# Performance work log

Measured on AMD Instinct MI355X. Metric: run time of the kernel, lower is better.

The kernel has to match this reference:

```python
import jax, jax.numpy as jnp
import numpy as np
import math

HEADS, LANDMARKS, PINV_ITERS, RES_K = 8, 256, 6, 33
DIM = 512


def layer_norm(x, g, b, eps=1e-5):
    mu = x.mean(-1, keepdims=True)
    var = ((x - mu) ** 2).mean(-1, keepdims=True)
    return (x - mu) * jax.lax.rsqrt(var + eps) * g + b


def iter_pinv(x, iters=PINV_ITERS):
    # Moore-Penrose pseudo-inverse via Newton-Schulz-like iteration (lucidrains nystrom-attention)
    ax = jnp.abs(x)
    z = jnp.swapaxes(x, -1, -2) / (jnp.max(ax.sum(-1)) * jnp.max(ax.sum(-2)))
    I = jnp.eye(x.shape[-1], dtype=x.dtype)
    for _ in range(iters):
        xz = x @ z
        z = 0.25 * z @ (13.0 * I - xz @ (15.0 * I - xz @ (7.0 * I - xz)))
    return z


def nystrom_attention(x, qkv_w, out_w, out_b, res_w):
    b, n, dim = x.shape
    h, m = HEADS, LANDMARKS
    d = dim // h
    pad = (m - n % m) % m
    xp = jnp.pad(x, ((0, 0), (pad, 0), (0, 0)))  # pad at sequence start (as in original)
    npad = n + pad
    qkv = xp @ qkv_w  # [b, npad, 3*dim]
    q, k, v = jnp.split(qkv, 3, axis=-1)
    q, k, v = (t.reshape(b, npad, h, d).transpose(0, 2, 1, 3) for t in (q, k, v))
    q = q * (d ** -0.5)
    l = npad // m
    q_l = q.reshape(b, h, m, l, d).mean(3)  # [b,h,m,d] landmarks
    k_l = k.reshape(b, h, m, l, d).mean(3)
    attn1 = jax.nn.softmax(jnp.einsum('bhid,bhjd->bhij', q, k_l), axis=-1)    # [b,h,npad,m]
    attn2 = jax.nn.softmax(jnp.einsum('bhid,bhjd->bhij', q_l, k_l), axis=-1)  # [b,h,m,m]
    attn3 = jax.nn.softmax(jnp.einsum('bhid,bhjd->bhij', q_l, k), axis=-1)    # [b,h,m,npad]
    out = (attn1 @ iter_pinv(attn2)) @ (attn3 @ v)  # [b,h,npad,d]
    # depthwise residual conv over sequence dim: v as NCHW = [b, heads, npad, d], kernel (33,1)
    res = jax.lax.conv_general_dilated(
        v, res_w, window_strides=(1, 1), padding=((RES_K // 2, RES_K // 2), (0, 0)),
        dimension_numbers=('NCHW', 'OIHW', 'NCHW'), feature_group_count=h)
    out = out + res
    out = out.transpose(0, 2, 1, 3).reshape(b, npad, dim)
    out = out @ out_w + out_b  # dropout is identity at eval
    return out[:, -n:]


def dwconv(x, w, b, k):
    y = jax.lax.conv_general_dilated(
        x, w, (1, 1), ((k // 2, k // 2), (k // 2, k // 2)),
        dimension_numbers=('NCHW', 'OIHW', 'NCHW'), feature_group_count=x.shape[1])
    return y + b[None, :, None, None]


def ppeg(x, H, W, w7, b7, w5, b5, w3, b3):
    B, _, C = x.shape
    cls_tok, feat = x[:, :1], x[:, 1:]
    cnn = feat.transpose(0, 2, 1).reshape(B, C, H, W)
    y = cnn + dwconv(cnn, w7, b7, 7) + dwconv(cnn, w5, b5, 5) + dwconv(cnn, w3, b3, 3)
    y = y.reshape(B, C, H * W).transpose(0, 2, 1)
    return jnp.concatenate([cls_tok, y], axis=1)


def _forward(features, fc1_w, fc1_b, cls_token,
             l1_norm_g, l1_norm_b, l1_qkv_w, l1_out_w, l1_out_b, l1_res_w,
             ppeg_w7, ppeg_b7, ppeg_w5, ppeg_b5, ppeg_w3, ppeg_b3,
             l2_norm_g, l2_norm_b, l2_qkv_w, l2_out_w, l2_out_b, l2_res_w,
             norm_g, norm_b, fc2_w, fc2_b):
    h = jax.nn.relu(features @ fc1_w + fc1_b)  # [B, N, 512]
    B, N, D = h.shape
    _H = _W = int(math.ceil(math.sqrt(N)))
    add_length = _H * _W - N
    h = jnp.concatenate([h, h[:, :add_length, :]], axis=1)  # square pad by wraparound
    h = jnp.concatenate([jnp.broadcast_to(cls_token, (B, 1, D)), h], axis=1)
    h = h + nystrom_attention(layer_norm(h, l1_norm_g, l1_norm_b), l1_qkv_w, l1_out_w, l1_out_b, l1_res_w)
    h = ppeg(h, _H, _W, ppeg_w7, ppeg_b7, ppeg_w5, ppeg_b5, ppeg_w3, ppeg_b3)
    h = h + nystrom_attention(layer_norm(h, l2_norm_g, l2_norm_b), l2_qkv_w, l2_out_w, l2_out_b, l2_res_w)
    h = layer_norm(h, norm_g, norm_b)[:, 0]
    return h @ fc2_w + fc2_b  # [B, num_classes]


def setup_inputs() -> dict:
    key = jax.random.key(0)
    ks = jax.random.split(key, 32)
    B, N, F, D = 2, 16000, 1024, DIM
    s = 0.02
    def rn(k, shape, scale=s):
        return jax.random.normal(k, shape, dtype=jnp.float32) * scale
    inp = {
        'features': jax.random.normal(ks[0], (B, N, F), dtype=jnp.float32),
        'fc1_w': rn(ks[1], (F, D)), 'fc1_b': jnp.zeros((D,), jnp.float32),
        'cls_token': rn(ks[2], (1, 1, D), 1.0),
        'l1_norm_g': jnp.ones((D,), jnp.float32), 'l1_norm_b': jnp.zeros((D,), jnp.float32),
        'l1_qkv_w': rn(ks[3], (D, 3 * D)),
        'l1_out_w': rn(ks[4], (D, D)), 'l1_out_b': jnp.zeros((D,), jnp.float32),
        'l1_res_w': rn(ks[5], (HEADS, 1, RES_K, 1)),
        'ppeg_w7': rn(ks[6], (D, 1, 7, 7)), 'ppeg_b7': jnp.zeros((D,), jnp.float32),
        'ppeg_w5': rn(ks[7], (D, 1, 5, 5)), 'ppeg_b5': jnp.zeros((D,), jnp.float32),
        'ppeg_w3': rn(ks[8], (D, 1, 3, 3)), 'ppeg_b3': jnp.zeros((D,), jnp.float32),
        'l2_norm_g': jnp.ones((D,), jnp.float32), 'l2_norm_b': jnp.zeros((D,), jnp.float32),
        'l2_qkv_w': rn(ks[9], (D, 3 * D)),
        'l2_out_w': rn(ks[10], (D, D)), 'l2_out_b': jnp.zeros((D,), jnp.float32),
        'l2_res_w': rn(ks[11], (HEADS, 1, RES_K, 1)),
        'norm_g': jnp.ones((D,), jnp.float32), 'norm_b': jnp.zeros((D,), jnp.float32),
        'fc2_w': rn(ks[12], (D, 1)), 'fc2_b': jnp.zeros((1,), jnp.float32),
    }
    return inp


def reference(features, fc1_w, fc1_b, cls_token,
              l1_norm_g, l1_norm_b, l1_qkv_w, l1_out_w, l1_out_b, l1_res_w,
              ppeg_w7, ppeg_b7, ppeg_w5, ppeg_b5, ppeg_w3, ppeg_b3,
              l2_norm_g, l2_norm_b, l2_qkv_w, l2_out_w, l2_out_b, l2_res_w,
              norm_g, norm_b, fc2_w, fc2_b):
    return _forward(features, fc1_w, fc1_b, cls_token,
                    l1_norm_g, l1_norm_b, l1_qkv_w, l1_out_w, l1_out_b, l1_res_w,
                    ppeg_w7, ppeg_b7, ppeg_w5, ppeg_b5, ppeg_w3, ppeg_b3,
                    l2_norm_g, l2_norm_b, l2_qkv_w, l2_out_w, l2_out_b, l2_res_w,
                    norm_g, norm_b, fc2_w, fc2_b)
```

## Files before the change

### kernel.cpp

```cpp
#include <hip/hip_runtime.h>
#include <math.h>

#define NTOK 16130
#define NPAD 16384
#define PADF 254
#define NB   2
#define DM   512
#define NH   8
#define HD   64
#define LM   256
#define SEG  64

typedef __attribute__((ext_vector_type(8))) short short8v;
typedef __attribute__((ext_vector_type(4))) float f32x4;
typedef __attribute__((ext_vector_type(2))) float f32x2;
typedef unsigned int u32;

__device__ __forceinline__ float wred_max(float v){
  #pragma unroll
  for(int o=32;o;o>>=1) v=fmaxf(v,__shfl_xor(v,o));
  return v;
}
__device__ __forceinline__ float wred_sum(float v){
  #pragma unroll
  for(int o=32;o;o>>=1) v+=__shfl_xor(v,o);
  return v;
}
__device__ __forceinline__ float block_max256(float v, float* s4){
  v=wred_max(v);
  if((threadIdx.x&63)==0) s4[threadIdx.x>>6]=v;
  __syncthreads();
  v=fmaxf(fmaxf(s4[0],s4[1]),fmaxf(s4[2],s4[3]));
  __syncthreads();
  return v;
}
__device__ __forceinline__ float block_sum256(float v, float* s4){
  v=wred_sum(v);
  if((threadIdx.x&63)==0) s4[threadIdx.x>>6]=v;
  __syncthreads();
  v=s4[0]+s4[1]+s4[2]+s4[3];
  __syncthreads();
  return v;
}
__device__ __forceinline__ unsigned short f2bf(float f){
  unsigned u=__float_as_uint(f);
  u = u + 0x7FFFu + ((u>>16)&1u);
  return (unsigned short)(u>>16);
}
__device__ __forceinline__ float bf2f(unsigned short u){
  return __uint_as_float(((unsigned)u)<<16);
}
__device__ __forceinline__ unsigned cvtpk(float a, float b){
  unsigned r;
  asm("v_cvt_pk_bf16_f32 %0, %1, %2" : "=v"(r) : "v"(a), "v"(b));
  return r;
}
__device__ __forceinline__ void gl16(const unsigned short* g, unsigned short* l){
  __builtin_amdgcn_global_load_lds(
      (const __attribute__((address_space(1))) u32*)(g),
      (__attribute__((address_space(3))) u32*)(l), 16, 0, 0);
}

__global__ void k_f2bf4(const float* __restrict__ x, unsigned short* __restrict__ y, int n4){
  int i=blockIdx.x*256+threadIdx.x; if(i>=n4) return;
  float4 v=((const float4*)x)[i];
  ushort4 r; r.x=f2bf(v.x); r.y=f2bf(v.y); r.z=f2bf(v.z); r.w=f2bf(v.w);
  ((ushort4*)y)[i]=r;
}
__global__ __launch_bounds__(256) void k_wconv_t(
    const float* __restrict__ W, unsigned short* __restrict__ Wt, int K, int N){
  __shared__ float T[32][33];
  int k0=blockIdx.x*32, n0=blockIdx.y*32;
  int t=threadIdx.x, r=t>>3, c4=(t&7)*4;
  float4 a=*(const float4*)(W+(size_t)(k0+r)*N + n0+c4);
  T[r][c4]=a.x; T[r][c4+1]=a.y; T[r][c4+2]=a.z; T[r][c4+3]=a.w;
  __syncthreads();
  ushort4 w;
  w.x=f2bf(T[c4+0][r]); w.y=f2bf(T[c4+1][r]);
  w.z=f2bf(T[c4+2][r]); w.w=f2bf(T[c4+3][r]);
  *(ushort4*)(Wt+(size_t)(n0+r)*K + k0+c4)=w;
}

template<int MODE, int ASRC>
__global__ __launch_bounds__(256) void k_mfma_gemm(
    const void* __restrict__ Ap, const unsigned short* __restrict__ Bt,
    int M, int N, int K,
    const float* __restrict__ bias,
    void* __restrict__ o0, void* __restrict__ o1, void* __restrict__ o2)
{
  __shared__ __align__(16) unsigned short Sh[128*64];
  int t=threadIdx.x;
  int bx=blockIdx.x, by=blockIdx.y;
  {
    int gx=gridDim.x; int wg=by*gx+bx; int nwg=gx*gridDim.y;
    int cpx=nwg>>3; int x2=(wg&7)*cpx+(wg>>3);
    by=x2/gx; bx=x2-by*gx;
  }
  int row0=by*128, col0=bx*128;
  int lane=t&63, w=t>>6, wr=w>>1, wc=w&1, lr=lane&15, kg=lane>>4;
  f32x4 acc[4][4];
  #pragma unroll
  for(int m=0;m<4;m++)
    #pragma unroll
    for(int n=0;n<4;n++) acc[m][n]=(f32x4){0.f,0.f,0.f,0.f};

  for(int k0=0;k0<K;k0+=32){
    __syncthreads();
    #pragma unroll
    for(int i=0;i<2;i++){
      int flat=i*256+t, r=flat>>2, k8=flat&3;
      int kofs=k0+k8*8;
      const unsigned short* asrc;
      if constexpr(ASRC==0){
        asrc=(const unsigned short*)Ap+(size_t)(row0+r)*K+kofs;
      } else {
        int rr2=row0+r; int bb=rr2>>14, ri=rr2&16383;
        int head=kofs>>6, dd=kofs&63;
        asrc=(const unsigned short*)Ap + (((size_t)bb*NH+head)*NPAD+ri)*HD + dd;
      }
      gl16(asrc, Sh+(size_t)flat*8);
      gl16(Bt+(size_t)(col0+r)*K+kofs, Sh+4096+(size_t)flat*8);
    }
    __syncthreads();
    short8v af[4], bf[4];
    #pragma unroll
    for(int m=0;m<4;m++) af[m]=*(const short8v*)(Sh+(wr*64+m*16+lr)*32 + kg*8);
    #pragma unroll
    for(int n=0;n<4;n++) bf[n]=*(const short8v*)(Sh+4096+(wc*64+n*16+lr)*32 + kg*8);
    #pragma unroll
    for(int m=0;m<4;m++)
      #pragma unroll
      for(int n=0;n<4;n++)
        acc[m][n]=__builtin_amdgcn_mfma_f32_16x16x32_bf16(af[m],bf[n],acc[m][n],0,0,0);
  }
  if constexpr(MODE==1){
    #pragma unroll
    for(int p=0;p<2;p++){
      __syncthreads();
      #pragma unroll
      for(int mm=0;mm<2;mm++){
        int m=2*p+mm;
        #pragma unroll
        for(int n=0;n<4;n++){
          int cc=wc*64+n*16+lr;
          int c=col0+cc;
          float sc=((c>>9)==0)?0.125f:1.f;
          #pragma unroll
          for(int j=0;j<4;j++){
            int lrow=wr*32+mm*16+kg*4+j;
            Sh[lrow*128+cc]=f2bf(acc[m][n][j]*sc);
          }
        }
      }
      __syncthreads();
      #pragma unroll
      for(int i=0;i<4;i++){
        int p2=i*256+t;
        int r2=p2>>4, ck=p2&15;
        int grow=row0+(r2>>5)*64+(2*p+((r2>>4)&1))*16+(r2&15);
        int bb=grow>>14, rr=grow&16383;
        int c=col0+ck*8;
        int which=c>>9, hcol=c&511, head=hcol>>6, dd=hcol&63;
        unsigned short* dst=(which==0)?(unsigned short*)o0:
                            (which==1)?(unsigned short*)o1:(unsigned short*)o2;
        *(short8v*)(dst + (((size_t)bb*NH+head)*NPAD+rr)*HD+dd) =
            *(const short8v*)(Sh + r2*128 + ck*8);
      }
    }
  } else {
    #pragma unroll
    for(int m=0;m<4;m++){
      int rbase=row0 + wr*64 + m*16 + kg*4;
      #pragma unroll
      for(int j=0;j<4;j++){
        int r=rbase+j;
        #pragma unroll
        for(int n=0;n<4;n++){
          int c=col0 + wc*64 + n*16 + lr;
          float val=acc[m][n][j];
          if(MODE==0){
            float* h=(float*)o0;
            int bb=(r>=16000)?1:0, ii=r-bb*16000;
            float vv=fmaxf(val+bias[c],0.f);
            h[((size_t)bb*NTOK + 1 + ii)*DM + c]=vv;
            if(ii<129) h[((size_t)bb*NTOK + 16001 + ii)*DM + c]=vv;
          } else {
            float* h=(float*)o0;
            int bb=r>>14, rr=r&16383;
            if(rr>=PADF)
              h[((size_t)bb*NTOK + (rr-PADF))*DM + c]+=val+bias[c];
          }
        }
      }
    }
  }
}

__global__ void k_cls(const float* __restrict__ cls, float* __restrict__ h){
  int t=blockIdx.x*256+threadIdx.x;
  if(t<2*DM) h[(size_t)(t>>9)*NTOK*DM + (t&511)]=cls[t&511];
}

__global__ __launch_bounds__(256) void k_lnpad(
    const float* __restrict__ h, const float* __restrict__ g,
    const float* __restrict__ bta, unsigned short* __restrict__ xln)
{
  int wid=blockIdx.x*4+(threadIdx.x>>6);
  int lane=threadIdx.x&63;
  int bb=wid>>14, i=wid&16383;
  unsigned short* dst=xln+(size_t)wid*DM+lane*8;
  if(i<PADF){
    ushort4 z=(ushort4){0,0,0,0};
    *(ushort4*)dst=z; *(ushort4*)(dst+4)=z;
    return;
  }
  const float* src=h+((size_t)bb*NTOK + (i-PADF))*DM + lane*8;
  float4 v0=*(const float4*)src;
  float4 v1=*(const float4*)(src+4);
  float x[8]={v0.x,v0.y,v0.z,v0.w,v1.x,v1.y,v1.z,v1.w};
  float s=0.f;
  #pragma unroll
  for(int k=0;k<8;k++) s+=x[k];
  float mu=wred_sum(s)*(1.f/512.f);
  float d[8]; float vs=0.f;
  #pragma unroll
  for(int k=0;k<8;k++){ d[k]=x[k]-mu; vs+=d[k]*d[k]; }
  float rst=rsqrtf(wred_sum(vs)*(1.f/512.f)+1e-5f);
  float4 g0=*(const float4*)(g+lane*8),   g1=*(const float4*)(g+lane*8+4);
  float4 b0=*(const float4*)(bta+lane*8), b1=*(const float4*)(bta+lane*8+4);
  float gg[8]={g0.x,g0.y,g0.z,g0.w,g1.x,g1.y,g1.z,g1.w};
  float bb8[8]={b0.x,b0.y,b0.z,b0.w,b1.x,b1.y,b1.z,b1.w};
  ushort4 w0,w1;
  w0.x=f2bf(d[0]*rst*gg[0]+bb8[0]); w0.y=f2bf(d[1]*rst*gg[1]+bb8[1]);
  w0.z=f2bf(d[2]*rst*gg[2]+bb8[2]); w0.w=f2bf(d[3]*rst*gg[3]+bb8[3]);
  w1.x=f2bf(d[4]*rst*gg[4]+bb8[4]); w1.y=f2bf(d[5]*rst*gg[5]+bb8[5]);
  w1.z=f2bf(d[6]*rst*gg[6]+bb8[6]); w1.w=f2bf(d[7]*rst*gg[7]+bb8[7]);
  *(ushort4*)dst=w0; *(ushort4*)(dst+4)=w1;
}

__global__ void k_lmean2(const unsigned short* __restrict__ qsrc,
                         const unsigned short* __restrict__ ksrc,
                         float* __restrict__ qlf, unsigned short* __restrict__ qlb_,
                         float* __restrict__ klf, unsigned short* __restrict__ klb_){
  int gid=blockIdx.x;
  const unsigned short* src; float* dstf; unsigned short* dstb;
  if(gid<4096){ src=qsrc; dstf=qlf; dstb=qlb_; }
  else        { src=ksrc; dstf=klf; dstb=klb_; gid-=4096; }
  int bh=gid>>8, s=gid&255, d=threadIdx.x;
  const unsigned short* p=src + (((size_t)bh*NPAD)+s*SEG)*HD + d;
  float acc=0.f;
  #pragma unroll
  for(int l=0;l<SEG;l++) acc+=bf2f(p[(size_t)l*HD]);
  float m=acc*(1.f/64.f);
  dstf[((size_t)bh*LM+s)*HD+d]=m;
  dstb[((size_t)bh*LM+s)*HD+d]=f2bf(m);
}

__global__ __launch_bounds__(256) void k_vtrans(
    const unsigned short* __restrict__ v, unsigned short* __restrict__ vt)
{
  __shared__ unsigned short tile[64][72];
  int kt=blockIdx.x, bh=blockIdx.y;
  int t=threadIdx.x;
  int r=t>>2, sgq=t&3;
  const short8v* src=(const short8v*)(v + ((size_t)bh*NPAD + kt*64 + r)*HD + sgq*16);
  *(short8v*)(&tile[r][sgq*16])  =src[0];
  *(short8v*)(&tile[r][sgq*16+8])=src[1];
  __syncthreads();
  int d=t>>2;
  union{unsigned short u[16]; short8v v8[2];} pk;
  #pragma unroll
  for(int i=0;i<16;i++) pk.u[i]=tile[sgq*16+i][d];
  short8v* dst=(short8v*)(vt + ((size_t)bh*HD + d)*NPAD + kt*64 + sgq*16);
  dst[0]=pk.v8[0]; dst[1]=pk.v8[1];
}

__global__ __launch_bounds__(256) void k_attn2(
    const float* __restrict__ ql, const float* __restrict__ kl,
    float* __restrict__ attn2,
    unsigned short* __restrict__ a2h, unsigned short* __restrict__ a2l)
{
  __shared__ float qrow[64]; __shared__ float s4[4];
  int bh=blockIdx.x>>8, i=blockIdx.x&255, j=threadIdx.x;
  if(j<64) qrow[j]=ql[((size_t)bh*LM+i)*HD+j];
  __syncthreads();
  const float* kp=kl+((size_t)bh*LM+j)*HD;
  float l=0.f;
  #pragma unroll
  for(int d=0;d<64;d++) l+=qrow[d]*kp[d];
  float m=block_max256(l,s4);
  float e=__expf(l-m);
  float s=block_sum256(e,s4);
  float pv=e/s;
  size_t o=((size_t)bh*LM+i)*LM+j;
  attn2[o]=pv;
  unsigned short hh=f2bf(pv);
  a2h[o]=hh; a2l[o]=f2bf(pv-bf2f(hh));
}

__global__ void k_colsumA(const float* __restrict__ x, float* __restrict__ partial){
  int bh=blockIdx.y, ic=blockIdx.x, j=threadIdx.x;
  const float* p=x+(size_t)bh*65536+(size_t)ic*16*256;
  float s=0.f;
  #pragma unroll
  for(int i=0;i<16;i++) s+=p[(size_t)i*256+j];
  partial[((size_t)bh*16+ic)*256+j]=s;
}
__global__ void k_colsumB(const float* __restrict__ partial, float* __restrict__ cs){
  int bh=blockIdx.x, j=threadIdx.x;
  float s=0.f;
  #pragma unroll
  for(int ic=0;ic<16;ic++) s+=partial[((size_t)bh*16+ic)*256+j];
  cs[bh*256+j]=s;
}
__global__ void k_pinvscale(const float* __restrict__ cs, float* __restrict__ scale){
  __shared__ float s4[4];
  float mc=-1e30f;
  for(int i=threadIdx.x;i<4096;i+=256) mc=fmaxf(mc,cs[i]);
  mc=block_max256(mc,s4);
  if(threadIdx.x==0) scale[0]=1.f/mc;
}
__global__ __launch_bounds__(256) void k_zinit_hl(
    const float* __restrict__ x, const float* __restrict__ scale,
    unsigned short* __restrict__ zh, unsigned short* __restrict__ zl,
    unsigned short* __restrict__ zth, unsigned short* __restrict__ ztl){
  __shared__ float T1[32][33], T2[32][33];
  int bh=blockIdx.x>>6, tile=blockIdx.x&63;
  int i0=(tile>>3)*32, j0=(tile&7)*32;
  int t=threadIdx.x, r=t>>3, c4=(t&7)*4;
  size_t base=(size_t)bh*65536;
  float4 a=*(const float4*)(x+base+(size_t)(i0+r)*256+j0+c4);
  float4 b=*(const float4*)(x+base+(size_t)(j0+r)*256+i0+c4);
  T1[r][c4]=a.x; T1[r][c4+1]=a.y; T1[r][c4+2]=a.z; T1[r][c4+3]=a.w;
  T2[r][c4]=b.x; T2[r][c4+1]=b.y; T2[r][c4+2]=b.z; T2[r][c4+3]=b.w;
  __syncthreads();
  float s=scale[0];
  size_t o=base+(size_t)(i0+r)*256+j0+c4;
  ushort4 nh,nl,th,tl;
  {
    float vn, vt; unsigned short hh;
    vn=T2[c4+0][r]*s; hh=f2bf(vn); nh.x=hh; nl.x=f2bf(vn-bf2f(hh));
    vn=T2[c4+1][r]*s; hh=f2bf(vn); nh.y=hh; nl.y=f2bf(vn-bf2f(hh));
    vn=T2[c4+2][r]*s; hh=f2bf(vn); nh.z=hh; nl.z=f2bf(vn-bf2f(hh));
    vn=T2[c4+3][r]*s; hh=f2bf(vn); nh.w=hh; nl.w=f2bf(vn-bf2f(hh));
    vt=T1[r][c4+0]*s; hh=f2bf(vt); th.x=hh; tl.x=f2bf(vt-bf2f(hh));
    vt=T1[r][c4+1]*s; hh=f2bf(vt); th.y=hh; tl.y=f2bf(vt-bf2f(hh));
    vt=T1[r][c4+2]*s; hh=f2bf(vt); th.z=hh; tl.z=f2bf(vt-bf2f(hh));
    vt=T1[r][c4+3]*s; hh=f2bf(vt); th.w=hh; tl.w=f2bf(vt-bf2f(hh));
  }
  *(ushort4*)(zh+o)=nh; *(ushort4*)(zl+o)=nl;
  *(ushort4*)(zth+o)=th; *(ushort4*)(ztl+o)=tl;
}

template<int MODE, int PREC>
__global__ __launch_bounds__(256) void k_bmm3(
    const unsigned short* __restrict__ Ah, const unsigned short* __restrict__ Al,
    const unsigned short* __restrict__ Bth, const unsigned short* __restrict__ Btl,
    const unsigned short* __restrict__ Xh, const unsigned short* __restrict__ Xl,
    unsigned short* __restrict__ Cnh, unsigned short* __restrict__ Cnl,
    unsigned short* __restrict__ Cth, unsigned short* __restrict__ Ctl,
    int Ndim)
{
  __shared__ unsigned short AsH[32*136], BsH[64*136];
  __shared__ unsigned short AsL[PREC?32*136:8], BsL[PREC?64*136:8];
  int bh=blockIdx.z;
  int n0=blockIdx.x*64, m0=blockIdx.y*32;
  int t=threadIdx.x, lane=t&63, w=t>>6;
  int c=lane&15, g=lane>>4;
  int wr=(w>>1)*16, wc=(w&1)*32;
  f32x4 acc[2];
  acc[0]=(f32x4){0.f,0.f,0.f,0.f};
  acc[1]=(f32x4){0.f,0.f,0.f,0.f};
  size_t Abase=(size_t)bh*65536;
  size_t Bbase=(size_t)bh*(size_t)Ndim*256;
  int r=t>>3, k16=(t&7)*16;
  const unsigned short* ApH =Ah +Abase+(size_t)(m0+r)*256+k16;
  const unsigned short* BpH0=Bth+Bbase+(size_t)(n0+r)*256+k16;
  const unsigned short* BpH1=Bth+Bbase+(size_t)(n0+32+r)*256+k16;
  const unsigned short* ApL =Al +Abase+(size_t)(m0+r)*256+k16;
  const unsigned short* BpL0=Btl+Bbase+(size_t)(n0+r)*256+k16;
  const unsigned short* BpL1=Btl+Bbase+(size_t)(n0+32+r)*256+k16;
  short8v rah[2],rbh0[2],rbh1[2], ral[2],rbl0[2],rbl1[2];
  #pragma unroll
  for(int i=0;i<2;i++){
    rah[i] =*(const short8v*)(ApH +i*8);
    rbh0[i]=*(const short8v*)(BpH0+i*8);
    rbh1[i]=*(const short8v*)(BpH1+i*8);
    if constexpr(PREC==1){
      ral[i] =*(const short8v*)(ApL +i*8);
      rbl0[i]=*(const short8v*)(BpL0+i*8);
      rbl1[i]=*(const short8v*)(BpL1+i*8);
    }
  }
  int k0=0;
  for(;;){
    __syncthreads();
    #pragma unroll
    for(int i=0;i<2;i++){
      *(short8v*)(AsH + r*136 + k16 + i*8)=rah[i];
      *(short8v*)(BsH + r*136 + k16 + i*8)=rbh0[i];
      *(short8v*)(BsH + (r+32)*136 + k16 + i*8)=rbh1[i];
      if constexpr(PREC==1){
        *(short8v*)(AsL + r*136 + k16 + i*8)=ral[i];
        *(short8v*)(BsL + r*136 + k16 + i*8)=rbl0[i];
        *(short8v*)(BsL + (r+32)*136 + k16 + i*8)=rbl1[i];
      }
    }
    __syncthreads();
    int kn=k0+128;
    if(kn<256){
      #pragma unroll
      for(int i=0;i<2;i++){
        rah[i] =*(const short8v*)(ApH +kn+i*8);
        rbh0[i]=*(const short8v*)(BpH0+kn+i*8);
        rbh1[i]=*(const short8v*)(BpH1+kn+i*8);
        if constexpr(PREC==1){
          ral[i] =*(const short8v*)(ApL +kn+i*8);
          rbl0[i]=*(const short8v*)(BpL0+kn+i*8);
          rbl1[i]=*(const short8v*)(BpL1+kn+i*8);
        }
      }
    }
    #pragma unroll
    for(int ks=0;ks<4;ks++){
      short8v af=*(const short8v*)(AsH+(wr+c)*136 + ks*32 + g*8);
      short8v alf;
      if constexpr(PREC==1) alf=*(const short8v*)(AsL+(wr+c)*136 + ks*32 + g*8);
      #pragma unroll
      for(int nt=0;nt<2;nt++){
        short8v bf=*(const short8v*)(BsH+(wc+nt*16+c)*136 + ks*32 + g*8);
        acc[nt]=__builtin_amdgcn_mfma_f32_16x16x32_bf16(af,bf,acc[nt],0,0,0);
        if constexpr(PREC==1){
          short8v blf=*(const short8v*)(BsL+(wc+nt*16+c)*136 + ks*32 + g*8);
          acc[nt]=__builtin_amdgcn_mfma_f32_16x16x32_bf16(af,blf,acc[nt],0,0,0);
          acc[nt]=__builtin_amdgcn_mfma_f32_16x16x32_bf16(alf,bf,acc[nt],0,0,0);
        }
      }
    }
    if(kn>=256) break;
    k0=kn;
  }
  int rb=m0+wr+g*4;
  #pragma unroll
  for(int nt=0;nt<2;nt++){
    int cc=n0+wc+nt*16+c;
    float vv[4];
    #pragma unroll
    for(int j=0;j<4;j++){
      float a=acc[nt][j];
      int rr=rb+j;
      if(MODE==1){
        float xv=bf2f(Xh[Abase+(size_t)rr*256+cc])+bf2f(Xl[Abase+(size_t)rr*256+cc]);
        a=(rr==cc?15.f:0.f)-7.f*xv+a;
      } else if(MODE==2){
        a=(rr==cc?13.f:0.f)-a;
      } else if(MODE==3){
        a*=0.25f;
      }
      vv[j]=a;
    }
    if(MODE==0||MODE==3){
      #pragma unroll
      for(int j=0;j<4;j++){
        unsigned short hh=f2bf(vv[j]);
        Cnh[Abase+(size_t)(rb+j)*256+cc]=hh;
        Cnl[Abase+(size_t)(rb+j)*256+cc]=f2bf(vv[j]-bf2f(hh));
      }
    }
    {
      ushort4 hv, lv;
      hv.x=f2bf(vv[0]); hv.y=f2bf(vv[1]); hv.z=f2bf(vv[2]); hv.w=f2bf(vv[3]);
      lv.x=f2bf(vv[0]-bf2f(hv.x)); lv.y=f2bf(vv[1]-bf2f(hv.y));
      lv.z=f2bf(vv[2]-bf2f(hv.z)); lv.w=f2bf(vv[3]-bf2f(hv.w));
      size_t co=((size_t)bh*Ndim+cc)*256+rb;
      *(ushort4*)(Cth+co)=hv;
      if(MODE!=4) *(ushort4*)(Ctl+co)=lv;
    }
  }
}

__global__ __launch_bounds__(512) void k_attn3m(
    const unsigned short* __restrict__ qlb,
    const unsigned short* __restrict__ kb,
    const unsigned short* __restrict__ vtb,
    float* __restrict__ pacc, float* __restrict__ pms)
{
  __shared__ unsigned short Ks[64*72];
  __shared__ unsigned short Vs[64*72];
  int ck=blockIdx.x, rh=blockIdx.y, bh=blockIdx.z;
  int t=threadIdx.x, lane=t&63, w=t>>6;
  int c=lane&15, g=lane>>4;
  int qrow0=rh*128 + w*16;
  short8v Qf[2];
  #pragma unroll
  for(int kw=0;kw<2;kw++)
    Qf[kw]=*(const short8v*)(qlb + ((size_t)bh*LM + qrow0 + c)*HD + kw*32 + g*8);
  f32x4 accO[4];
  float mrun=-3e38f, srun=0.f;
  #pragma unroll
  for(int d=0;d<4;d++) accO[d]=(f32x4){0.f,0.f,0.f,0.f};
  int sr=t>>3, sgk=t&7;
  for(int sc=0;sc<16;++sc){
    int key0=ck*1024 + sc*64;
    __syncthreads();
    *(short8v*)(Ks + sr*72 + sgk*8) =
      *(const short8v*)(kb + ((size_t)bh*NPAD + key0 + sr)*HD + sgk*8);
    *(short8v*)(Vs + sr*72 + sgk*8) =
      *(const short8v*)(vtb + ((size_t)bh*HD + sr)*NPAD + key0 + sgk*8);
    __syncthreads();
    f32x4 s[4];
    #pragma unroll
    for(int mt=0;mt<4;mt++){
      short8v a0=*(const short8v*)(Ks + (mt*16+c)*72 + g*8);
      short8v a1=*(const short8v*)(Ks + (mt*16+c)*72 + 32 + g*8);
      f32x4 z=(f32x4){0.f,0.f,0.f,0.f};
      z=__builtin_amdgcn_mfma_f32_16x16x32_bf16(a0,Qf[0],z,0,0,0);
      z=__builtin_amdgcn_mfma_f32_16x16x32_bf16(a1,Qf[1],z,0,0,0);
      s[mt]=z;
    }
    unsigned U[4][2];
    {
      float cm=-3e38f;
      #pragma unroll
      for(int mt=0;mt<4;mt++)
        #pragma unroll
        for(int j=0;j<4;j++) cm=fmaxf(cm,s[mt][j]);
      cm=fmaxf(cm,__shfl_xor(cm,16));
      cm=fmaxf(cm,__shfl_xor(cm,32));
      float mnew=fmaxf(mrun,cm);
      float f=__expf(mrun-mnew);
      mrun=mnew;
      float ps=0.f;
      #pragma unroll
      for(int mt=0;mt<4;mt++){
        float p0=__expf(s[mt][0]-mnew);
        float p1=__expf(s[mt][1]-mnew);
        float p2=__expf(s[mt][2]-mnew);
        float p3=__expf(s[mt][3]-mnew);
        ps+=p0+p1+p2+p3;
        U[mt][0]=cvtpk(p0,p1);
        U[mt][1]=cvtpk(p2,p3);
      }
      ps+=__shfl_xor(ps,16); ps+=__shfl_xor(ps,32);
      srun=srun*f+ps;
      #pragma unroll
      for(int d=0;d<4;d++){
        accO[d][0]*=f; accO[d][1]*=f; accO[d][2]*=f; accO[d][3]*=f;
      }
    }
    #pragma unroll
    for(int kw=0;kw<2;kw++){
      union{unsigned u[4]; short8v v;} pk;
      #pragma unroll
      for(int wd=0;wd<4;wd++){
        int sl=c+16*(((g&1)<<1)+(wd>>1));
        unsigned va=(unsigned)__shfl((int)U[kw*2  ][wd&1],sl);
        unsigned vb=(unsigned)__shfl((int)U[kw*2+1][wd&1],sl);
        pk.u[wd]=(lane>=32)?vb:va;
      }
      #pragma unroll
      for(int d=0;d<4;d++){
        short8v vf=*(const short8v*)(Vs + (d*16+c)*72 + kw*32 + g*8);
        accO[d]=__builtin_amdgcn_mfma_f32_16x16x32_bf16(vf,pk.v,accO[d],0,0,0);
      }
    }
  }
  size_t pb=((size_t)bh*16+ck)*LM;
  int q=qrow0+c;
  #pragma unroll
  for(int d=0;d<4;d++)
    *(f32x4*)(pacc + (pb+q)*HD + d*16 + g*4)=accO[d];
  if(g==0){ pms[(pb+q)*2]=mrun; pms[(pb+q)*2+1]=srun; }
}
__global__ __launch_bounds__(256) void k_attn3vc(
    const float* __restrict__ pacc, const float* __restrict__ pms,
    unsigned short* __restrict__ a3vth, unsigned short* __restrict__ a3vtl)
{
  int gid=blockIdx.x*4+(threadIdx.x>>6);
  int bh=gid>>8, row=gid&255, lane=threadIdx.x&63;
  float M=-3e38f;
  float ms[16], ss[16];
  #pragma unroll
  for(int c=0;c<16;c++){
    size_t pb=((size_t)bh*16+c)*LM+row;
    ms[c]=pms[pb*2]; ss[c]=pms[pb*2+1];
    M=fmaxf(M,ms[c]);
  }
  float S=0.f,a=0.f;
  #pragma unroll
  for(int c=0;c<16;c++){
    float f=__expf(ms[c]-M);
    S+=ss[c]*f;
    a+=pacc[(((size_t)bh*16+c)*LM+row)*HD+lane]*f;
  }
  float v=a/S;
  unsigned short hi=f2bf(v);
  a3vth[((size_t)bh*HD+lane)*LM+row]=hi;
  a3vtl[((size_t)bh*HD+lane)*LM+row]=f2bf(v-bf2f(hi));
}

__global__ __launch_bounds__(512) void k_attn1m(
    const unsigned short* __restrict__ qb,
    const unsigned short* __restrict__ klb,
    const unsigned short* __restrict__ w2t,
    unsigned short* __restrict__ aohb)
{
  __shared__ unsigned short klS[256*72];
  __shared__ unsigned short w2S[64*264];
  int qt=blockIdx.x, bh=blockIdx.y;
  int t=threadIdx.x, lane=t&63, w=t>>6;
  int c=lane&15, g=lane>>4;
  {
    int r=t>>1, hf=t&1;
    const short8v* s=(const short8v*)(klb + ((size_t)bh*LM+r)*HD + hf*32);
    short8v* d=(short8v*)(klS + r*72 + hf*32);
    d[0]=s[0]; d[1]=s[1]; d[2]=s[2]; d[3]=s[3];
    int r2=t>>3, sg2=t&7;
    const short8v* s2=(const short8v*)(w2t + ((size_t)bh*HD+r2)*LM + sg2*32);
    short8v* d2=(short8v*)(w2S + r2*264 + sg2*32);
    d2[0]=s2[0]; d2[1]=s2[1]; d2[2]=s2[2]; d2[3]=s2[3];
  }
  __syncthreads();
  int q0=qt*256 + w*32;
  #pragma unroll
  for(int n=0;n<2;n++){
    const unsigned short* qrow=qb + ((size_t)bh*NPAD + q0 + n*16 + c)*HD;
    short8v qf0=*(const short8v*)(qrow + g*8);
    short8v qf1=*(const short8v*)(qrow + 32 + g*8);
    f32x4 s[16];
    #pragma unroll
    for(int mt=0;mt<16;mt++){
      short8v a0=*(const short8v*)(klS + (mt*16+c)*72 + g*8);
      short8v a1=*(const short8v*)(klS + (mt*16+c)*72 + 32 + g*8);
      f32x4 z=(f32x4){0.f,0.f,0.f,0.f};
      z=__builtin_amdgcn_mfma_f32_16x16x32_bf16(a0,qf0,z,0,0,0);
      z=__builtin_amdgcn_mfma_f32_16x16x32_bf16(a1,qf1,z,0,0,0);
      s[mt]=z;
    }
    float M=-3e38f;
    #pragma unroll
    for(int mt=0;mt<16;mt++)
      #pragma unroll
      for(int j=0;j<4;j++) M=fmaxf(M,s[mt][j]);
    M=fmaxf(M,__shfl_xor(M,16));
    M=fmaxf(M,__shfl_xor(M,32));
    float sum=0.f;
    unsigned U[16][2];
    #pragma unroll
    for(int mt=0;mt<16;mt++){
      float p0=__expf(s[mt][0]-M);
      float p1=__expf(s[mt][1]-M);
      float p2=__expf(s[mt][2]-M);
      float p3=__expf(s[mt][3]-M);
      sum+=p0+p1+p2+p3;
      U[mt][0]=cvtpk(p0,p1);
      U[mt][1]=cvtpk(p2,p3);
    }
    sum+=__shfl_xor(sum,16); sum+=__shfl_xor(sum,32);
    float inv=1.f/sum;
    f32x4 accO[4];
    #pragma unroll
    for(int d=0;d<4;d++) accO[d]=(f32x4){0.f,0.f,0.f,0.f};
    #pragma unroll
    for(int kw=0;kw<8;kw++){
      union{unsigned u[4]; short8v v;} pk;
      #pragma unroll
      for(int wd=0;wd<4;wd++){
        int sl=c+16*(((g&1)<<1)+(wd>>1));
        unsigned va=(unsigned)__shfl((int)U[kw*2  ][wd&1],sl);
        unsigned vb=(unsigned)__shfl((int)U[kw*2+1][wd&1],sl);
        pk.u[wd]=(lane>=32)?vb:va;
      }
      #pragma unroll
      for(int d=0;d<4;d++){
        short8v vf=*(const short8v*)(w2S + (d*16+c)*264 + kw*32 + g*8);
        accO[d]=__builtin_amdgcn_mfma_f32_16x16x32_bf16(vf,pk.v,accO[d],0,0,0);
      }
    }
    int q=q0+n*16+c;
    #pragma unroll
    for(int d=0;d<4;d++){
      f32x4 o=accO[d];
      uint2 pk2;
      pk2.x=cvtpk(o[0]*inv, o[1]*inv);
      pk2.y=cvtpk(o[2]*inv, o[3]*inv);
      *(uint2*)(aohb + ((size_t)bh*NPAD+q)*HD + d*16 + g*4)=pk2;
    }
  }
}

__global__ __launch_bounds__(256) void k_resconv2(
    const unsigned short* __restrict__ vt, const float* __restrict__ rw,
    unsigned short* __restrict__ aohb){
  int bx=blockIdx.x, bh=blockIdx.y;
  int t=threadIdx.x, d=t&63, g=t>>6;
  int i0=bx*32+g*8;
  int hh=bh&7;
  const unsigned short* vr=vt + ((size_t)bh*HD + d)*NPAD;
  float wv[40];
  int start=i0-16;
  if(start>=0 && start+40<=NPAD){
    #pragma unroll
    for(int b=0;b<5;b++){
      short8v v8=*(const short8v*)(vr+start+b*8);
      #pragma unroll
      for(int j=0;j<8;j++) wv[b*8+j]=bf2f((unsigned short)v8[j]);
    }
  } else {
    #pragma unroll
    for(int t2=0;t2<40;t2++){
      int src=start+t2;
      wv[t2]=(src>=0&&src<NPAD)?bf2f(vr[src]):0.f;
    }
  }
  const float* wt=rw+hh*33;
  #pragma unroll
  for(int p=0;p<8;p++){
    float a=0.f;
    #pragma unroll
    for(int tk=0;tk<33;tk++) a+=wv[p+tk]*wt[tk];
    size_t o=((size_t)bh*NPAD+i0+p)*HD+d;
    aohb[o]=f2bf(bf2f(aohb[o])+a);
  }
}

__global__ void k_wprep(const float* __restrict__ w7, const float* __restrict__ b7,
                        const float* __restrict__ w5, const float* __restrict__ b5,
                        const float* __restrict__ w3, const float* __restrict__ b3,
                        unsigned short* __restrict__ wcat){
  int t=blockIdx.x*256+threadIdx.x;
  if(t>=50*512) return;
  int r=t>>9, c=t&511;
  float v;
  if(r<49){
    int ky=r/7, kx=r%7;
    v=w7[(size_t)c*49+r];
    if(ky>=1&&ky<=5&&kx>=1&&kx<=5) v+=w5[(size_t)c*25+(ky-1)*5+(kx-1)];
    if(ky>=2&&ky<=4&&kx>=2&&kx<=4) v+=w3[(size_t)c*9+(ky-2)*3+(kx-2)];
  } else {
    v=b7[c]+b5[c]+b3[c];
  }
  wcat[t]=f2bf(v);
}

__global__ __launch_bounds__(256,4) void k_ppeg4(
    const float* __restrict__ src, const unsigned short* __restrict__ wcat,
    float* __restrict__ dst)
{
  __shared__ float patch[32][198];
  __shared__ float wsf[50][32];
  int bx=blockIdx.x;
  int cz=blockIdx.y, bb=blockIdx.z;
  int t=threadIdx.x, c=t&31, g=t>>5;
  int ty0=(bx>>4)*8, tx0=(bx&15)*8;
  const float* base=src+((size_t)bb*NTOK+1)*DM + cz*32 + c;
  #pragma unroll
  for(int i=0;i<25;i++){
    int p=g+8*i;
    if(p<196){
      int py=p/14, px=p%14;
      int yy=ty0-3+py, xx=tx0-3+px;
      float v=0.f;
      if(yy>=0&&yy<127&&xx>=0&&xx<127) v=base[(size_t)(yy*127+xx)*DM];
      patch[c][p]=v;
    }
  }
  #pragma unroll
  for(int i=0;i<7;i++){
    int r=g+8*i; if(r<50) wsf[r][c]=bf2f(wcat[(size_t)r*DM + cz*32 + c]);
  }
  __syncthreads();
  float bias=wsf[49][c];
  f32x2 acc2[4];
  #pragma unroll
  for(int j=0;j<4;j++){
    acc2[j][0]=patch[c][(g+3)*14+(j+3)]+bias;
    acc2[j][1]=patch[c][(g+3)*14+(j+7)]+bias;
  }
  #pragma unroll
  for(int ky=0;ky<7;ky++){
    float win[14];
    #pragma unroll
    for(int x2=0;x2<7;x2++){
      f32x2 wp=*(const f32x2*)(&patch[c][(g+ky)*14+2*x2]);
      win[2*x2]=wp[0]; win[2*x2+1]=wp[1];
    }
    #pragma unroll
    for(int kx=0;kx<7;kx++){
      float wv=wsf[ky*7+kx][c];
      f32x2 w2={wv,wv};
      #pragma unroll
      for(int j=0;j<4;j++){
        f32x2 v2={win[j+kx],win[j+4+kx]};
        acc2[j]=__builtin_elementwise_fma(v2,w2,acc2[j]);
      }
    }
  }
  int y=ty0+g;
  if(y<127){
    #pragma unroll
    for(int j=0;j<4;j++){
      int x=tx0+j;
      if(x<127)
        dst[((size_t)bb*NTOK+1+(size_t)(y*127+x))*DM + cz*32 + c]=acc2[j][0];
      int x4=tx0+j+4;
      if(x4<127)
        dst[((size_t)bb*NTOK+1+(size_t)(y*127+x4))*DM + cz*32 + c]=acc2[j][1];
    }
  }
}

__global__ void k_cpcls(const float* __restrict__ h, float* __restrict__ dst){
  int t=blockIdx.x*256+threadIdx.x;
  if(t<2*DM) dst[(size_t)(t>>9)*NTOK*DM + (t&511)]=h[(size_t)(t>>9)*NTOK*DM + (t&511)];
}

__global__ __launch_bounds__(256) void k_final(
    const float* __restrict__ h, const float* __restrict__ g, const float* __restrict__ bta,
    const float* __restrict__ w, const float* __restrict__ fb, float* __restrict__ out)
{
  int bb=blockIdx.x, t=threadIdx.x;
  const float* src=h+(size_t)bb*NTOK*DM;
  float x0=src[t], x1=src[t+256];
  __shared__ float s4[4];
  float mu=block_sum256(x0+x1,s4)*(1.f/512.f);
  float d0=x0-mu, d1=x1-mu;
  float var=block_sum256(d0*d0+d1*d1,s4)*(1.f/512.f);
  float rst=rsqrtf(var+1e-5f);
  float y0=d0*rst*g[t]+bta[t], y1=d1*rst*g[t+256]+bta[t+256];
  float dot=block_sum256(y0*w[t]+y1*w[t+256],s4);
  if(t==0) out[bb]=dot+fb[0];
}

extern "C" void kernel_launch(void* const* d_in, const int* in_sizes, int n_in,
                              void* d_out, int out_size, void* d_ws, size_t ws_size,
                              hipStream_t stream){
  (void)in_sizes; (void)n_in; (void)out_size; (void)ws_size;
  const float* features=(const float*)d_in[0];
  const float* fc1_w  =(const float*)d_in[1];
  const float* fc1_b  =(const float*)d_in[2];
  const float* cls_tok=(const float*)d_in[3];
  const float* fc2_w  =(const float*)d_in[24];
  const float* fc2_b  =(const float*)d_in[25];
  float* out=(float*)d_out;

  char* wp=(char*)d_ws;
  auto allocB=[&](size_t bytes)->char*{
    char* p=wp; wp+=((bytes+255)/256)*256; return p;
  };
  float* h    =(float*)allocB((size_t)NB*NTOK*DM*4);
  float* h2   =(float*)allocB((size_t)NB*NTOK*DM*4);
  unsigned short* vb  =(unsigned short*)allocB((size_t)NB*NPAD*DM*2);
  unsigned short* xlnb=(unsigned short*)allocB((size_t)NB*NPAD*DM*2);
  unsigned short* qb  =(unsigned short*)allocB((size_t)NB*NPAD*DM*2);
  unsigned short* kb  =(unsigned short*)allocB((size_t)NB*NPAD*DM*2);
  unsigned short* vtb =(unsigned short*)allocB((size_t)NB*NPAD*DM*2);
  unsigned short* aohb=(unsigned short*)allocB((size_t)NB*NPAD*DM*2);
  unsigned short* wtf=(unsigned short*)allocB((size_t)512*1024*2);
  unsigned short* wtq=(unsigned short*)allocB((size_t)1536*512*2);
  unsigned short* wtp=(unsigned short*)allocB((size_t)512*512*2);
  float* ql =(float*)allocB((size_t)16*LM*HD*4);
  float* kl =(float*)allocB((size_t)16*LM*HD*4);
  unsigned short* qlb=(unsigned short*)allocB((size_t)16*LM*HD*2);
  unsigned short* klb=(unsigned short*)allocB((size_t)16*LM*HD*2);
  float* attn2=(float*)allocB((size_t)16*LM*LM*4);
  unsigned short* a2h=(unsigned short*)allocB((size_t)16*LM*LM*2);
  unsigned short* a2l=(unsigned short*)allocB((size_t)16*LM*LM*2);
  unsigned short* zb[8];
  for(int i=0;i<8;i++) zb[i]=(unsigned short*)allocB((size_t)16*LM*LM*2);
  unsigned short* Abh=(unsigned short*)allocB((size_t)16*LM*LM*2);
  unsigned short* Abl=(unsigned short*)allocB((size_t)16*LM*LM*2);
  unsigned short* Abth=(unsigned short*)allocB((size_t)16*LM*LM*2);
  unsigned short* Abtl=(unsigned short*)allocB((size_t)16*LM*LM*2);
  unsigned short* Ubth=(unsigned short*)allocB((size_t)16*LM*LM*2);
  unsigned short* Ubtl=(unsigned short*)allocB((size_t)16*LM*LM*2);
  unsigned short* Tbth=(unsigned short*)allocB((size_t)16*LM*LM*2);
  unsigned short* Tbtl=(unsigned short*)allocB((size_t)16*LM*LM*2);
  unsigned short* a3vth=(unsigned short*)allocB((size_t)16*HD*LM*2);
  unsigned short* a3vtl=(unsigned short*)allocB((size_t)16*HD*LM*2);
  unsigned short* w2t=(unsigned short*)allocB((size_t)16*HD*LM*2);
  float* pacc=(float*)allocB((size_t)16*16*LM*HD*4);
  float* pms =(float*)allocB((size_t)16*16*LM*2*4);
  float* cs  =(float*)allocB(4096*4);
  float* scl =(float*)allocB(64*4);

  auto nystrom=[&](float* hbuf, const float* ng, const float* nbias, const float* qkvw,
                   const float* outw, const float* outb, const float* resw){
    k_lnpad<<<NB*NPAD/4,256,0,stream>>>(hbuf, ng, nbias, xlnb);
    k_wconv_t<<<dim3(16,48),256,0,stream>>>(qkvw, wtq, 512, 1536);
    k_mfma_gemm<1,0><<<dim3(12,256),256,0,stream>>>(xlnb, wtq, 32768,1536,512,
                                                    nullptr, qb, kb, vb);
    k_lmean2<<<8192,64,0,stream>>>(qb, kb, ql, qlb, kl, klb);
    k_vtrans<<<dim3(256,16),256,0,stream>>>(vb, vtb);
    k_attn2<<<4096,256,0,stream>>>(ql, kl, attn2, a2h, a2l);
    k_colsumA<<<dim3(16,16),256,0,stream>>>(attn2, pacc);
    k_colsumB<<<16,256,0,stream>>>(pacc, cs);
    k_pinvscale<<<1,256,0,stream>>>(cs, scl);
    k_zinit_hl<<<1024,256,0,stream>>>(attn2, scl, zb[0],zb[1],zb[2],zb[3]);
    unsigned short *zch=zb[0],*zcl=zb[1],*zcth=zb[2],*zctl=zb[3];
    unsigned short *znh=zb[4],*znl=zb[5],*znth=zb[6],*zntl=zb[7];
    for(int it=0;it<6;it++){
      if(it<5){
        k_bmm3<0,0><<<dim3(4,8,16),256,0,stream>>>(a2h,a2l, zcth,zctl, nullptr,nullptr,
                                                   Abh,Abl, Abth,Abtl, 256);
        k_bmm3<1,0><<<dim3(4,8,16),256,0,stream>>>(Abh,Abl, Abth,Abtl, Abh,Abl,
                                                   nullptr,nullptr, Ubth,Ubtl, 256);
        k_bmm3<2,0><<<dim3(4,8,16),256,0,stream>>>(Abh,Abl, Ubth,Ubtl, nullptr,nullptr,
                                                   nullptr,nullptr, Tbth,Tbtl, 256);
        k_bmm3<3,0><<<dim3(4,8,16),256,0,stream>>>(zch,zcl, Tbth,Tbtl, nullptr,nullptr,
                                                   znh,znl, znth,zntl, 256);
      } else {
        k_bmm3<0,1><<<dim3(4,8,16),256,0,stream>>>(a2h,a2l, zcth,zctl, nullptr,nullptr,
                                                   Abh,Abl, Abth,Abtl, 256);
        k_bmm3<1,1><<<dim3(4,8,16),256,0,stream>>>(Abh,Abl, Abth,Abtl, Abh,Abl,
                                                   nullptr,nullptr, Ubth,Ubtl, 256);
        k_bmm3<2,1><<<dim3(4,8,16),256,0,stream>>>(Abh,Abl, Ubth,Ubtl, nullptr,nullptr,
                                                   nullptr,nullptr, Tbth,Tbtl, 256);
        k_bmm3<3,1><<<dim3(4,8,16),256,0,stream>>>(zch,zcl, Tbth,Tbtl, nullptr,nullptr,
                                                   znh,znl, znth,zntl, 256);
      }
      unsigned short* tp;
      tp=zch; zch=znh; znh=tp;  tp=zcl; zcl=znl; znl=tp;
      tp=zcth; zcth=znth; znth=tp;  tp=zctl; zctl=zntl; zntl=tp;
    }
    k_attn3m<<<dim3(16,2,16),512,0,stream>>>(qlb, kb, vtb, pacc, pms);
    k_attn3vc<<<1024,256,0,stream>>>(pacc, pms, a3vth, a3vtl);
    k_bmm3<4,1><<<dim3(1,8,16),256,0,stream>>>(zch,zcl, a3vth,a3vtl, nullptr,nullptr,
                                               nullptr,nullptr, w2t,nullptr, 64);
    k_attn1m<<<dim3(64,16),512,0,stream>>>(qb, klb, w2t, aohb);
    k_resconv2<<<dim3(512,16),256,0,stream>>>(vtb, resw, aohb);
    k_wconv_t<<<dim3(16,16),256,0,stream>>>(outw, wtp, 512, 512);
    k_mfma_gemm<2,3><<<dim3(4,256),256,0,stream>>>(aohb, wtp, 32768,512,512,
                                                   outb, hbuf, nullptr, nullptr);
  };

  unsigned short* featbf=(unsigned short*)h2;
  k_f2bf4<<<32000,256,0,stream>>>(features, featbf, 32000*1024/4);
  k_wconv_t<<<dim3(32,16),256,0,stream>>>(fc1_w, wtf, 1024, 512);
  k_mfma_gemm<0,0><<<dim3(4,250),256,0,stream>>>(featbf, wtf, 32000,512,1024,
                                                 fc1_b, h, nullptr, nullptr);
  k_cls<<<4,256,0,stream>>>(cls_tok, h);

  nystrom(h, (const float*)d_in[4],(const float*)d_in[5],(const float*)d_in[6],
          (const float*)d_in[7],(const float*)d_in[8],(const float*)d_in[9]);

  {
    unsigned short* wcat=(unsigned short*)attn2;
    k_wprep<<<100,256,0,stream>>>(
        (const float*)d_in[10],(const float*)d_in[11],
        (const float*)d_in[12],(const float*)d_in[13],
        (const float*)d_in[14],(const float*)d_in[15], wcat);
    k_cpcls<<<4,256,0,stream>>>(h, h2);
    k_ppeg4<<<dim3(256,16,2),256,0,stream>>>(h, wcat, h2);
  }

  nystrom(h2, (const float*)d_in[16],(const float*)d_in[17],(const float*)d_in[18],
          (const float*)d_in[19],(const float*)d_in[20],(const float*)d_in[21]);

  k_final<<<2,256,0,stream>>>(h2,(const float*)d_in[22],(const float*)d_in[23],
                              fc2_w, fc2_b, out);
}
```

Baseline: 1.196 ms.

## Fuse pinv Newton-Schulz stages into one persistent kernel with grid barriers

Replaces the four separate bmm launches per pseudo-inverse iteration with one persistent kernel of 256 blocks using 64x64 tiles. The four matmul modes are separated by atomic grid-wide barriers instead of kernel boundaries. This removes launch overhead and inter-kernel gaps across 24 small launches per layer. It relies on all 256 blocks being co-resident, otherwise the barrier deadlocks. The residual conv now reads v in row layout with strided scalar loads instead of the transposed copy, giving up vectorized loads.

```diff
diff --git a/kernel.cpp b/kernel.cpp
--- a/kernel.cpp
+++ b/kernel.cpp
@@ -350,6 +350,133 @@
   }
   *(ushort4*)(zh+o)=nh; *(ushort4*)(zl+o)=nl;
   *(ushort4*)(zth+o)=th; *(ushort4*)(ztl+o)=tl;
+}
+
+__device__ __forceinline__ void gridbar(unsigned* bar, unsigned target){
+  __threadfence();
+  __syncthreads();
+  if(threadIdx.x==0){
+    __hip_atomic_fetch_add(bar,1u,__ATOMIC_RELEASE,__HIP_MEMORY_SCOPE_AGENT);
+    while(__hip_atomic_load(bar,__ATOMIC_ACQUIRE,__HIP_MEMORY_SCOPE_AGENT)<target)
+      __builtin_amdgcn_s_sleep(2);
+  }
+  __syncthreads();
+}
+
+template<int PREC>
+__global__ __launch_bounds__(256) void k_pinv_iter(
+    const unsigned short* __restrict__ a2h_, const unsigned short* __restrict__ a2l_,
+    const unsigned short* __restrict__ zcth, const unsigned short* __restrict__ zctl,
+    const unsigned short* __restrict__ zch,  const unsigned short* __restrict__ zcl,
+    unsigned short* __restrict__ Abh, unsigned short* __restrict__ Abl,
+    unsigned short* __restrict__ Abth, unsigned short* __restrict__ Abtl,
+    unsigned short* __restrict__ Ubth, unsigned short* __restrict__ Ubtl,
+    unsigned short* __restrict__ Tbth, unsigned short* __restrict__ Tbtl,
+    unsigned short* __restrict__ znh, unsigned short* __restrict__ znl,
+    unsigned short* __restrict__ znth, unsigned short* __restrict__ zntl,
+    unsigned* __restrict__ bar)
+{
+  __shared__ unsigned short AsH[64*136], BsH[64*136];
+  __shared__ unsigned short AsL[PREC?64*136:8], BsL[PREC?64*136:8];
+  int bh=blockIdx.z;
+  int n0=blockIdx.x*64, m0=blockIdx.y*64;
+  int t=threadIdx.x, lane=t&63, w=t>>6;
+  int c=lane&15, g=lane>>4;
+  int wr=(w>>1)*32, wc=(w&1)*32;
+  size_t base=(size_t)bh*65536;
+  int slr=t>>2, slk=(t&3)*32;
+
+  for(int mode=0;mode<4;mode++){
+    const unsigned short *Ah,*Al,*Bh,*Bl;
+    if(mode==0){ Ah=a2h_; Al=a2l_; Bh=zcth; Bl=zctl; }
+    else if(mode==1){ Ah=Abh; Al=Abl; Bh=Abth; Bl=Abtl; }
+    else if(mode==2){ Ah=Abh; Al=Abl; Bh=Ubth; Bl=Ubtl; }
+    else { Ah=zch; Al=zcl; Bh=Tbth; Bl=Tbtl; }
+    f32x4 acc[2][2];
+    #pragma unroll
+    for(int i=0;i<2;i++)
+      #pragma unroll
+      for(int j=0;j<2;j++) acc[i][j]=(f32x4){0.f,0.f,0.f,0.f};
+    for(int kb=0;kb<256;kb+=128){
+      __syncthreads();
+      #pragma unroll
+      for(int i=0;i<4;i++){
+        *(short8v*)(AsH+slr*136+slk+i*8)=
+            *(const short8v*)(Ah+base+(size_t)(m0+slr)*256+kb+slk+i*8);
+        *(short8v*)(BsH+slr*136+slk+i*8)=
+            *(const short8v*)(Bh+base+(size_t)(n0+slr)*256+kb+slk+i*8);
+        if constexpr(PREC==1){
+          *(short8v*)(AsL+slr*136+slk+i*8)=
+              *(const short8v*)(Al+base+(size_t)(m0+slr)*256+kb+slk+i*8);
+          *(short8v*)(BsL+slr*136+slk+i*8)=
+              *(const short8v*)(Bl+base+(size_t)(n0+slr)*256+kb+slk+i*8);
+        }
+      }
+      __syncthreads();
+      #pragma unroll
+      for(int ks=0;ks<4;ks++){
+        #pragma unroll
+        for(int mt=0;mt<2;mt++){
+          short8v af=*(const short8v*)(AsH+(wr+mt*16+c)*136+ks*32+g*8);
+          short8v alf;
+          if constexpr(PREC==1) alf=*(const short8v*)(AsL+(wr+mt*16+c)*136+ks*32+g*8);
+          #pragma unroll
+          for(int nt=0;nt<2;nt++){
+            short8v bf=*(const short8v*)(BsH+(wc+nt*16+c)*136+ks*32+g*8);
+            acc[mt][nt]=__builtin_amdgcn_mfma_f32_16x16x32_bf16(af,bf,acc[mt][nt],0,0,0);
+            if constexpr(PREC==1){
+              short8v blf=*(const short8v*)(BsL+(wc+nt*16+c)*136+ks*32+g*8);
+              acc[mt][nt]=__builtin_amdgcn_mfma_f32_16x16x32_bf16(af,blf,acc[mt][nt],0,0,0);
+              acc[mt][nt]=__builtin_amdgcn_mfma_f32_16x16x32_bf16(alf,bf,acc[mt][nt],0,0,0);
+            }
+          }
+        }
+      }
+    }
+    unsigned short *Cnh=nullptr,*Cnl=nullptr,*Cth,*Ctl;
+    if(mode==0){ Cnh=Abh; Cnl=Abl; Cth=Abth; Ctl=Abtl; }
+    else if(mode==1){ Cth=Ubth; Ctl=Ubtl; }
+    else if(mode==2){ Cth=Tbth; Ctl=Tbtl; }
+    else { Cnh=znh; Cnl=znl; Cth=znth; Ctl=zntl; }
+    #pragma unroll
+    for(int mt=0;mt<2;mt++)
+      #pragma unroll
+      for(int nt=0;nt<2;nt++){
+        int rb=m0+wr+mt*16+g*4;
+        int cc=n0+wc+nt*16+c;
+        float vv[4];
+        #pragma unroll
+        for(int j=0;j<4;j++){
+          float a=acc[mt][nt][j];
+          int rr=rb+j;
+          if(mode==1){
+            float xv=bf2f(Abh[base+(size_t)rr*256+cc])+bf2f(Abl[base+(size_t)rr*256+cc]);
+            a=(rr==cc?15.f:0.f)-7.f*xv+a;
+          } else if(mode==2){
+            a=(rr==cc?13.f:0.f)-a;
+          } else if(mode==3){
+            a*=0.25f;
+          }
+          vv[j]=a;
+        }
+        if(Cnh){
+          #pragma unroll
+          for(int j=0;j<4;j++){
+            unsigned short hh=f2bf(vv[j]);
+            Cnh[base+(size_t)(rb+j)*256+cc]=hh;
+            Cnl[base+(size_t)(rb+j)*256+cc]=f2bf(vv[j]-bf2f(hh));
+          }
+        }
+        ushort4 hv, lv;
+        hv.x=f2bf(vv[0]); hv.y=f2bf(vv[1]); hv.z=f2bf(vv[2]); hv.w=f2bf(vv[3]);
+        lv.x=f2bf(vv[0]-bf2f(hv.x)); lv.y=f2bf(vv[1]-bf2f(hv.y));
+        lv.z=f2bf(vv[2]-bf2f(hv.z)); lv.w=f2bf(vv[3]-bf2f(hv.w));
+        size_t co=base+(size_t)cc*256+rb;
+        *(ushort4*)(Cth+co)=hv;
+        *(ushort4*)(Ctl+co)=lv;
+      }
+    if(mode<3) gridbar(bar,(unsigned)((mode+1)*256));
+  }
 }
 
 template<int MODE, int PREC>
@@ -690,28 +817,19 @@
 }
 
 __global__ __launch_bounds__(256) void k_resconv2(
-    const unsigned short* __restrict__ vt, const float* __restrict__ rw,
+    const unsigned short* __restrict__ v, const float* __restrict__ rw,
     unsigned short* __restrict__ aohb){
   int bx=blockIdx.x, bh=blockIdx.y;
   int t=threadIdx.x, d=t&63, g=t>>6;
   int i0=bx*32+g*8;
   int hh=bh&7;
-  const unsigned short* vr=vt + ((size_t)bh*HD + d)*NPAD;
+  const unsigned short* vr=v + (size_t)bh*NPAD*HD + d;
   float wv[40];
   int start=i0-16;
-  if(start>=0 && start+40<=NPAD){
-    #pragma unroll
-    for(int b=0;b<5;b++){
-      short8v v8=*(const short8v*)(vr+start+b*8);
-      #pragma unroll
-      for(int j=0;j<8;j++) wv[b*8+j]=bf2f((unsigned short)v8[j]);
-    }
-  } else {
-    #pragma unroll
-    for(int t2=0;t2<40;t2++){
-      int src=start+t2;
-      wv[t2]=(src>=0&&src<NPAD)?bf2f(vr[src]):0.f;
-    }
+  #pragma unroll
+  for(int t2=0;t2<40;t2++){
+    int src=start+t2;
+    wv[t2]=(src>=0&&src<NPAD)?bf2f(vr[(size_t)src*HD]):0.f;
   }
   const float* wt=rw+hh*33;
   #pragma unroll
@@ -883,9 +1001,13 @@
   float* pms =(float*)allocB((size_t)16*16*LM*2*4);
   float* cs  =(float*)allocB(4096*4);
   float* scl =(float*)allocB(64*4);
+  unsigned* bars=(unsigned*)allocB(64);
+
+  hipMemsetAsync(bars, 0, 64, stream);
 
   auto nystrom=[&](float* hbuf, const float* ng, const float* nbias, const float* qkvw,
-                   const float* outw, const float* outb, const float* resw){
+                   const float* outw, const float* outb, const float* resw,
+                   unsigned* barp){
     k_lnpad<<<NB*NPAD/4,256,0,stream>>>(hbuf, ng, nbias, xlnb);
     k_wconv_t<<<dim3(16,48),256,0,stream>>>(qkvw, wtq, 512, 1536);
     k_mfma_gemm<1,0><<<dim3(12,256),256,0,stream>>>(xlnb, wtq, 32768,1536,512,
@@ -901,23 +1023,15 @@
     unsigned short *znh=zb[4],*znl=zb[5],*znth=zb[6],*zntl=zb[7];
     for(int it=0;it<6;it++){
       if(it<5){
-        k_bmm3<0,0><<<dim3(4,8,16),256,0,stream>>>(a2h,a2l, zcth,zctl, nullptr,nullptr,
-                                                   Abh,Abl, Abth,Abtl, 256);
-        k_bmm3<1,0><<<dim3(4,8,16),256,0,stream>>>(Abh,Abl, Abth,Abtl, Abh,Abl,
-                                                   nullptr,nullptr, Ubth,Ubtl, 256);
-        k_bmm3<2,0><<<dim3(4,8,16),256,0,stream>>>(Abh,Abl, Ubth,Ubtl, nullptr,nullptr,
-                                                   nullptr,nullptr, Tbth,Tbtl, 256);
-        k_bmm3<3,0><<<dim3(4,8,16),256,0,stream>>>(zch,zcl, Tbth,Tbtl, nullptr,nullptr,
-                                                   znh,znl, znth,zntl, 256);
+        k_pinv_iter<0><<<dim3(4,4,16),256,0,stream>>>(
+            a2h,a2l, zcth,zctl, zch,zcl,
+            Abh,Abl,Abth,Abtl, Ubth,Ubtl, Tbth,Tbtl,
+            znh,znl,znth,zntl, barp+it);
       } else {
-        k_bmm3<0,1><<<dim3(4,8,16),256,0,stream>>>(a2h,a2l, zcth,zctl, nullptr,nullptr,
-                                                   Abh,Abl, Abth,Abtl, 256);
-        k_bmm3<1,1><<<dim3(4,8,16),256,0,stream>>>(Abh,Abl, Abth,Abtl, Abh,Abl,
-                                                   nullptr,nullptr, Ubth,Ubtl, 256);
-        k_bmm3<2,1><<<dim3(4,8,16),256,0,stream>>>(Abh,Abl, Ubth,Ubtl, nullptr,nullptr,
-                                                   nullptr,nullptr, Tbth,Tbtl, 256);
-        k_bmm3<3,1><<<dim3(4,8,16),256,0,stream>>>(zch,zcl, Tbth,Tbtl, nullptr,nullptr,
-                                                   znh,znl, znth,zntl, 256);
+        k_pinv_iter<1><<<dim3(4,4,16),256,0,stream>>>(
+            a2h,a2l, zcth,zctl, zch,zcl,
+            Abh,Abl,Abth,Abtl, Ubth,Ubtl, Tbth,Tbtl,
+            znh,znl,znth,zntl, barp+it);
       }
       unsigned short* tp;
       tp=zch; zch=znh; znh=tp;  tp=zcl; zcl=znl; znl=tp;
@@ -928,7 +1042,7 @@
     k_bmm3<4,1><<<dim3(1,8,16),256,0,stream>>>(zch,zcl, a3vth,a3vtl, nullptr,nullptr,
                                                nullptr,nullptr, w2t,nullptr, 64);
     k_attn1m<<<dim3(64,16),512,0,stream>>>(qb, klb, w2t, aohb);
-    k_resconv2<<<dim3(512,16),256,0,stream>>>(vtb, resw, aohb);
+    k_resconv2<<<dim3(512,16),256,0,stream>>>(vb, resw, aohb);
     k_wconv_t<<<dim3(16,16),256,0,stream>>>(outw, wtp, 512, 512);
     k_mfma_gemm<2,3><<<dim3(4,256),256,0,stream>>>(aohb, wtp, 32768,512,512,
                                                    outb, hbuf, nullptr, nullptr);
@@ -942,7 +1056,7 @@
   k_cls<<<4,256,0,stream>>>(cls_tok, h);
 
   nystrom(h, (const float*)d_in[4],(const float*)d_in[5],(const float*)d_in[6],
-          (const float*)d_in[7],(const float*)d_in[8],(const float*)d_in[9]);
+          (const float*)d_in[7],(const float*)d_in[8],(const float*)d_in[9], bars);
 
   {
     unsigned short* wcat=(unsigned short*)attn2;
@@ -955,7 +1069,7 @@
   }
 
   nystrom(h2, (const float*)d_in[16],(const float*)d_in[17],(const float*)d_in[18],
-          (const float*)d_in[19],(const float*)d_in[20],(const float*)d_in[21]);
+          (const float*)d_in[19],(const float*)d_in[20],(const float*)d_in[21], bars+6);
 
   k_final<<<2,256,0,stream>>>(h2,(const float*)d_in[22],(const float*)d_in[23],
                               fc2_w, fc2_b, out);
```

Result: slower. 2.959 ms (+147.3%).
